# Kernel optimization log

Measured on AMD Instinct MI355X. Metric: run time of the kernel, lower is better.

The kernel has to match this reference:

```python
import jax, jax.numpy as jnp
import numpy as np

B, S, E, H = 2, 2048, 1024, 16
D = E // H  # dim per head


def setup_inputs() -> dict:
    key = jax.random.key(0)
    ks = jax.random.split(key, 13)
    sc = 1.0 / np.sqrt(E)
    inp = {
        "query": jax.random.normal(ks[0], (B, S, E), jnp.float32),
        "key": jax.random.normal(ks[1], (B, S, E), jnp.float32),
        "value": jax.random.normal(ks[2], (B, S, E), jnp.float32),
        "mask": jax.random.randint(ks[3], (B, S, S), 0, 2, jnp.int32),
        "Wq": jax.random.normal(ks[4], (E, E), jnp.float32) * sc,
        "bq": jnp.zeros((E,), jnp.float32),
        "Wk": jax.random.normal(ks[5], (E, E), jnp.float32) * sc,
        "bk": jnp.zeros((E,), jnp.float32),
        "Wv": jax.random.normal(ks[6], (E, E), jnp.float32) * sc,
        "bv": jnp.zeros((E,), jnp.float32),
        "Wo": jax.random.normal(ks[7], (E, E), jnp.float32) * sc,
        "bo": jnp.zeros((E,), jnp.float32),
    }
    return inp


def _split_heads(x):
    # [B, S, E] -> [B, H, S, D]
    return x.reshape(B, S, H, D).transpose(0, 2, 1, 3)


def reference(query, key, value, mask, Wq, bq, Wk, bk, Wv, bv, Wo, bo):
    q = _split_heads(query @ Wq.T + bq)
    k = _split_heads(key @ Wk.T + bk)
    v = _split_heads(value @ Wv.T + bv)

    dk = k.shape[-1]
    # scores: [B, H, Sq, Sk]
    scores = jnp.einsum("bhqd,bhkd->bhqk", q / jnp.sqrt(jnp.asarray(dk, q.dtype)), k)
    # mask broadcast over heads: [B, 1, Sq, Sk]; masked positions get -1e9
    scores = jnp.where(mask[:, None, :, :] == 0, jnp.asarray(-1e9, scores.dtype), scores)
    # fp32 softmax (dropout is identity in eval mode)
    attn = jax.nn.softmax(scores.astype(jnp.float32), axis=-1).astype(q.dtype)
    out = jnp.einsum("bhqk,bhkd->bhqd", attn, v)
    out = out.transpose(0, 2, 1, 3).reshape(B, S, E)
    return out @ Wo.T + bo
```

## Files before the change

kernel.cpp:

```cpp
#include <hip/hip_runtime.h>
#include <hip/hip_bf16.h>
#include <stdint.h>


typedef __bf16 bf16x8 __attribute__((ext_vector_type(8)));
typedef __bf16 bf16x4 __attribute__((ext_vector_type(4)));
typedef float  f32x4  __attribute__((ext_vector_type(4)));
typedef unsigned int u32x4 __attribute__((ext_vector_type(4)));

#define MFMA16(a, b, c) __builtin_amdgcn_mfma_f32_16x16x32_bf16((a), (b), (c), 0, 0, 0)

#if __has_builtin(__builtin_amdgcn_exp2f)
#define EXP2(x) __builtin_amdgcn_exp2f(x)
#else
#define EXP2(x) exp2f(x)
#endif

static constexpr int kB = 2, kS = 2048, kE = 1024, kH = 16, kD = 64;
static constexpr int kM = kB * kS;
static constexpr int kMaskWordsPerRow = kS / 64;
static constexpr float kLog2e = 1.4426950408889634f;

__device__ __forceinline__ void gload_lds16(const void* g, void* l) {
  __builtin_amdgcn_global_load_lds(
      (const __attribute__((address_space(1))) unsigned int*)g,
      (__attribute__((address_space(3))) unsigned int*)l, 16, 0, 0);
}

__device__ __forceinline__ unsigned pack_bf16x2(float a, float b) {
  unsigned short lo = __builtin_bit_cast(unsigned short, (__bf16)a);
  unsigned short hi = __builtin_bit_cast(unsigned short, (__bf16)b);
  return (unsigned)lo | ((unsigned)hi << 16);
}

static constexpr int kCvtBlocks = 1664;

__global__ __launch_bounds__(256) void cvt_pack_kernel(
    const float* __restrict__ q, const float* __restrict__ k, const float* __restrict__ v,
    const float* __restrict__ wq, const float* __restrict__ wk,
    const float* __restrict__ wv, const float* __restrict__ wo,
    const int* __restrict__ mask,
    __bf16* __restrict__ qb, __bf16* __restrict__ kb, __bf16* __restrict__ vb,
    __bf16* __restrict__ wqb, __bf16* __restrict__ wkb,
    __bf16* __restrict__ wvb, __bf16* __restrict__ wob,
    unsigned long long* __restrict__ mw) {
  const int bid = blockIdx.x;
  if (bid < 1216) {
    const float* src; __bf16* dst; int n8, t0, stride;
    if (bid < 960) {
      const int seg = bid / 320, sb = bid - seg * 320;
      src = (seg == 0) ? q : (seg == 1) ? k : v;
      dst = (seg == 0) ? qb : (seg == 1) ? kb : vb;
      n8 = (kM * kE) >> 3;
      t0 = sb * 256 + threadIdx.x;
      stride = 320 * 256;
    } else {
      const int wseg = (bid - 960) >> 6, sb = (bid - 960) & 63;
      src = (wseg == 0) ? wq : (wseg == 1) ? wk : (wseg == 2) ? wv : wo;
      dst = (wseg == 0) ? wqb : (wseg == 1) ? wkb : (wseg == 2) ? wvb : wob;
      n8 = (kE * kE) >> 3;
      t0 = sb * 256 + threadIdx.x;
      stride = 64 * 256;
    }
    for (int i = t0; i < n8; i += stride) {
      float4 f0 = ((const float4*)src)[2 * i];
      float4 f1 = ((const float4*)src)[2 * i + 1];
      bf16x8 o = {(__bf16)f0.x, (__bf16)f0.y, (__bf16)f0.z, (__bf16)f0.w,
                  (__bf16)f1.x, (__bf16)f1.y, (__bf16)f1.z, (__bf16)f1.w};
      ((bf16x8*)dst)[i] = o;
    }
    return;
  }
  const int lane = threadIdx.x & 63;
  const int wid = ((bid - 1216) * 4 + (threadIdx.x >> 6));
  const int nwords = kB * kS * kMaskWordsPerRow;
  const int stride4 = 1792 * 4;
  for (int w = wid * 4; w < nwords; w += stride4) {
    const int v0 = mask[(size_t)(w + 0) * 64 + lane];
    const int v1 = mask[(size_t)(w + 1) * 64 + lane];
    const int v2 = mask[(size_t)(w + 2) * 64 + lane];
    const int v3 = mask[(size_t)(w + 3) * 64 + lane];
    const unsigned long long b0 = __ballot(v0 != 0);
    const unsigned long long b1 = __ballot(v1 != 0);
    const unsigned long long b2 = __ballot(v2 != 0);
    const unsigned long long b3 = __ballot(v3 != 0);
    if (lane == 0) {
      ulonglong2 lo = {b0, b1}, hi = {b2, b3};
      *(ulonglong2*)&mw[w] = lo;
      *(ulonglong2*)&mw[w + 2] = hi;
    }
  }
}

__global__ __launch_bounds__(256) void gemm_bt(
    const __bf16* __restrict__ A0, const __bf16* __restrict__ A1, const __bf16* __restrict__ A2,
    const __bf16* __restrict__ W0, const __bf16* __restrict__ W1, const __bf16* __restrict__ W2,
    const float* __restrict__ b0, const float* __restrict__ b1, const float* __restrict__ b2,
    __bf16* __restrict__ O0, __bf16* __restrict__ O1, __bf16* __restrict__ O2) {
  const int z = blockIdx.z;
  const __bf16* A = (z == 0) ? A0 : (z == 1) ? A1 : A2;
  const __bf16* W = (z == 0) ? W0 : (z == 1) ? W1 : W2;
  const float* bias = (z == 0) ? b0 : (z == 1) ? b1 : b2;
  __bf16* OutB = (z == 0) ? O0 : (z == 1) ? O1 : O2;
  const float scale = (z == 0) ? 0.125f * kLog2e : 1.0f;

  const int n0 = blockIdx.x * 128;
  const int m0 = blockIdx.y * 128;
  const int tid = threadIdx.x;
  const int wave = tid >> 6, lane = tid & 63;
  const int g = lane >> 4, qi = lane & 15;
  const int wm = wave >> 1, wn = wave & 1;

  __shared__ __align__(16) __bf16 As[128 * 32];
  __shared__ __align__(16) __bf16 Bs[128 * 32];
  __shared__ __align__(16) __bf16 Ts[64 * 136];

  f32x4 acc[4][4];
#pragma unroll
  for (int i = 0; i < 4; ++i)
#pragma unroll
    for (int jj = 0; jj < 4; ++jj) acc[i][jj] = (f32x4){0.f, 0.f, 0.f, 0.f};

  for (int k0 = 0; k0 < kE; k0 += 32) {
#pragma unroll
    for (int jj = 0; jj < 2; ++jj) {
      const int c = jj * 256 + tid;
      const int r = c >> 2, sl = c & 3;
      gload_lds16(&A[(size_t)(m0 + r) * kE + k0 + sl * 8], &As[c * 8]);
      gload_lds16(&W[(size_t)(n0 + r) * kE + k0 + sl * 8], &Bs[c * 8]);
    }
    __syncthreads();

    bf16x8 af[4], bfr[4];
#pragma unroll
    for (int mi = 0; mi < 4; ++mi)
      af[mi] = *(const bf16x8*)&As[(wm * 64 + mi * 16 + qi) * 32 + g * 8];
#pragma unroll
    for (int nj = 0; nj < 4; ++nj)
      bfr[nj] = *(const bf16x8*)&Bs[(wn * 64 + nj * 16 + qi) * 32 + g * 8];
#pragma unroll
    for (int mi = 0; mi < 4; ++mi)
#pragma unroll
      for (int nj = 0; nj < 4; ++nj)
        acc[mi][nj] = MFMA16(af[mi], bfr[nj], acc[mi][nj]);
    __syncthreads();
  }

  if (z == 2) {
    const int bb = m0 >> 11, ss0 = m0 & 2047;
#pragma unroll
    for (int half = 0; half < 2; ++half) {
      __syncthreads();
      if (wn == half) {
#pragma unroll
        for (int nj = 0; nj < 4; ++nj) {
          const int dl = nj * 16 + qi;
          const float bn = bias[n0 + half * 64 + dl];
#pragma unroll
          for (int mi = 0; mi < 4; ++mi) {
            const int srow = wm * 64 + mi * 16 + g * 4;
            bf16x4 o;
#pragma unroll
            for (int r = 0; r < 4; ++r) o[r] = (__bf16)(acc[mi][nj][r] + bn);
            *(bf16x4*)&Ts[dl * 136 + srow] = o;
          }
        }
      }
      __syncthreads();
      const int drow = tid >> 2, sc = (tid & 3) * 32;
      const int head = (n0 + half * 64) >> 6;
      __bf16* dst = OutB + (((size_t)bb * kH + head) * kD + drow) * kS + ss0 + sc;
#pragma unroll
      for (int jj = 0; jj < 4; ++jj) {
        bf16x8 vv = *(const bf16x8*)&Ts[drow * 136 + sc + jj * 8];
        *(bf16x8*)&dst[jj * 8] = vv;
      }
    }
    return;
  }

#pragma unroll
  for (int nj = 0; nj < 4; ++nj) {
    const int ncol = n0 + wn * 64 + nj * 16 + qi;
    const float bn = bias[ncol];
    const int hh = ncol >> 6, dd = ncol & 63;
#pragma unroll
    for (int mi = 0; mi < 4; ++mi) {
#pragma unroll
      for (int r = 0; r < 4; ++r) {
        const int mrow = m0 + wm * 64 + mi * 16 + g * 4 + r;
        const float vv = (acc[mi][nj][r] + bn) * scale;
        const int bb = mrow >> 11, ss = mrow & 2047;
        OutB[((((size_t)bb * kH + hh) * kS + ss) << 6) + dd] = (__bf16)vv;
      }
    }
  }
}

__global__ __launch_bounds__(256) void gemm_out64(
    const __bf16* __restrict__ A, const __bf16* __restrict__ W,
    const float* __restrict__ bias, float* __restrict__ OF) {
  const int n0 = blockIdx.x * 64;
  const int m0 = blockIdx.y * 128;
  const int tid = threadIdx.x;
  const int wave = tid >> 6, lane = tid & 63;
  const int g = lane >> 4, qi = lane & 15;
  const int wm = wave >> 1, wn = wave & 1;

  __shared__ __align__(16) __bf16 As[128 * 32];
  __shared__ __align__(16) __bf16 Bs[64 * 32];

  f32x4 acc[4][2];
#pragma unroll
  for (int i = 0; i < 4; ++i)
#pragma unroll
    for (int jj = 0; jj < 2; ++jj) acc[i][jj] = (f32x4){0.f, 0.f, 0.f, 0.f};

  for (int k0 = 0; k0 < kE; k0 += 32) {
#pragma unroll
    for (int jj = 0; jj < 2; ++jj) {
      const int c = jj * 256 + tid;
      const int r = c >> 2, sl = c & 3;
      gload_lds16(&A[(size_t)(m0 + r) * kE + k0 + sl * 8], &As[c * 8]);
    }
    {
      const int r = tid >> 2, sl = tid & 3;
      gload_lds16(&W[(size_t)(n0 + r) * kE + k0 + sl * 8], &Bs[tid * 8]);
    }
    __syncthreads();

    bf16x8 af[4], bfr[2];
#pragma unroll
    for (int mi = 0; mi < 4; ++mi)
      af[mi] = *(const bf16x8*)&As[(wm * 64 + mi * 16 + qi) * 32 + g * 8];
#pragma unroll
    for (int nj = 0; nj < 2; ++nj)
      bfr[nj] = *(const bf16x8*)&Bs[(wn * 32 + nj * 16 + qi) * 32 + g * 8];
#pragma unroll
    for (int mi = 0; mi < 4; ++mi)
#pragma unroll
      for (int nj = 0; nj < 2; ++nj)
        acc[mi][nj] = MFMA16(af[mi], bfr[nj], acc[mi][nj]);
    __syncthreads();
  }

#pragma unroll
  for (int nj = 0; nj < 2; ++nj) {
    const int ncol = n0 + wn * 32 + nj * 16 + qi;
    const float bn = bias[ncol];
#pragma unroll
    for (int mi = 0; mi < 4; ++mi)
#pragma unroll
      for (int r = 0; r < 4; ++r) {
        const int mrow = m0 + wm * 64 + mi * 16 + g * 4 + r;
        OF[(size_t)mrow * kE + ncol] = acc[mi][nj][r] + bn;
      }
  }
}

__global__ __launch_bounds__(512, 4) void attn_kernel(
    const __bf16* __restrict__ Qh, const __bf16* __restrict__ Kh,
    const __bf16* __restrict__ Vt, const unsigned long long* __restrict__ mw,
    __bf16* __restrict__ Ob) {
  const int tid = threadIdx.x;
  const int wave = tid >> 6, lane = tid & 63;
  const int g = lane >> 4, qi = lane & 15;
  const int id = blockIdx.x;
  const int xcd = id & 7, j = id >> 3;
  const int bh = xcd * 4 + (j >> 4);
  const int qb = j & 15;
  const int b = bh >> 4, h = bh & 15;

  __shared__ __align__(16) __bf16 Ks[2][128 * 64];
  __shared__ __align__(16) __bf16 Vs[2][64 * 128];

  const __bf16* Qp = Qh + (size_t)bh * kS * kD;
  const __bf16* Kp = Kh + (size_t)bh * kS * kD;
  const __bf16* Vp = Vt + (size_t)bh * kD * kS;

  const int q0 = qb * 128 + wave * 16 + qi;
  const unsigned long long* M0 = mw + (size_t)(b * kS + q0) * kMaskWordsPerRow;

  const bf16x8 qf0 = *(const bf16x8*)&Qp[(size_t)q0 * kD + g * 8];
  const bf16x8 qf1 = *(const bf16x8*)&Qp[(size_t)q0 * kD + 32 + g * 8];

  f32x4 acc[4];
#pragma unroll
  for (int f = 0; f < 4; ++f) acc[f] = (f32x4){0.f, 0.f, 0.f, 0.f};
  float den = 0.f;
  const float ninf = __builtin_bit_cast(float, 0xff800000u);

  auto stage = [&](int buf, int kv0) {
#pragma unroll
    for (int jj = 0; jj < 2; ++jj) {
      const int c = jj * 512 + tid;
      const int kr = c >> 3, ksl = c & 7;
      gload_lds16(&Kp[(size_t)(kv0 + kr) * kD + (ksl ^ (kr & 7)) * 8],
                  &Ks[buf][c * 8]);
      const int vr = c >> 4, vsl = c & 15;
      gload_lds16(&Vp[(size_t)vr * kS + kv0 + (vsl ^ (vr & 7)) * 8],
                  &Vs[buf][c * 8]);
    }
  };

  stage(0, 0);
  __syncthreads();

  const int sw = qi & 7;
  for (int t = 0; t < 16; ++t) {
    const int cur = t & 1;
    if (t < 15) stage(cur ^ 1, (t + 1) * 128);
    const ulonglong2 wpair = *(const ulonglong2*)&M0[2 * t];
#pragma unroll
    for (int u = 0; u < 2; ++u) {
      const unsigned long long w = u ? wpair.y : wpair.x;
      const unsigned wlo = (unsigned)(w >> (g * 4));
      const unsigned whi = (unsigned)(w >> (32 + g * 4));
      const unsigned wf[4] = {wlo, wlo >> 16, whi, whi >> 16};

      float p[16];
      __builtin_amdgcn_s_setprio(1);
#pragma unroll
      for (int f = 0; f < 4; ++f) {
        const int r = u * 64 + f * 16 + qi;
        const bf16x8 k0 = *(const bf16x8*)&Ks[cur][r * 64 + ((g ^ sw) * 8)];
        const bf16x8 k1 = *(const bf16x8*)&Ks[cur][r * 64 + (((4 + g) ^ sw) * 8)];
        f32x4 st = (f32x4){0.f, 0.f, 0.f, 0.f};
        st = MFMA16(k0, qf0, st);
        st = MFMA16(k1, qf1, st);
#pragma unroll
        for (int r4 = 0; r4 < 4; ++r4)
          p[4 * f + r4] = (wf[f] & (1u << r4)) ? st[r4] : ninf;
      }
      __builtin_amdgcn_s_setprio(0);

#pragma unroll
      for (int i = 0; i < 16; ++i) {
        p[i] = EXP2(p[i]);
        den += p[i];
      }

      unsigned pk[4][2];
#pragma unroll
      for (int f = 0; f < 4; ++f) {
        pk[f][0] = pack_bf16x2(p[4 * f + 0], p[4 * f + 1]);
        pk[f][1] = pack_bf16x2(p[4 * f + 2], p[4 * f + 3]);
      }
#pragma unroll
      for (int c = 0; c < 2; ++c) {
        unsigned bw[4];
#pragma unroll
        for (int t4 = 0; t4 < 4; ++t4) {
          const int src = qi + 16 * ((t4 >> 1) + 2 * (g & 1));
          const int vA = __shfl((int)pk[2 * c + 0][t4 & 1], src);
          const int vB = __shfl((int)pk[2 * c + 1][t4 & 1], src);
          bw[t4] = (g >= 2) ? (unsigned)vB : (unsigned)vA;
        }
        const u32x4 tmp = {bw[0], bw[1], bw[2], bw[3]};
        const bf16x8 pb = __builtin_bit_cast(bf16x8, tmp);
        __builtin_amdgcn_s_setprio(1);
#pragma unroll
        for (int f = 0; f < 4; ++f) {
          const int rd = f * 16 + qi;
          const int slot = (u * 8 + c * 4 + g) ^ sw;
          const bf16x8 vfr = *(const bf16x8*)&Vs[cur][rd * 128 + slot * 8];
          acc[f] = MFMA16(vfr, pb, acc[f]);
        }
        __builtin_amdgcn_s_setprio(0);
      }
    }
    __syncthreads();
  }

  den += __shfl_xor(den, 16);
  den += __shfl_xor(den, 32);
  const float rinv = 1.0f / den;
  __bf16* Op = Ob + (size_t)(b * kS + q0) * kE + h * kD;
#pragma unroll
  for (int f = 0; f < 4; ++f) {
    ushort4 o;
    o.x = __builtin_bit_cast(unsigned short, (__bf16)(acc[f][0] * rinv));
    o.y = __builtin_bit_cast(unsigned short, (__bf16)(acc[f][1] * rinv));
    o.z = __builtin_bit_cast(unsigned short, (__bf16)(acc[f][2] * rinv));
    o.w = __builtin_bit_cast(unsigned short, (__bf16)(acc[f][3] * rinv));
    *(ushort4*)&Op[f * 16 + g * 4] = o;
  }
}

extern "C" void kernel_launch(void* const* d_in, const int* in_sizes, int n_in,
                              void* d_out, int out_size, void* d_ws, size_t ws_size,
                              hipStream_t stream) {
  (void)in_sizes; (void)n_in; (void)out_size; (void)ws_size;
  const float* q  = (const float*)d_in[0];
  const float* k  = (const float*)d_in[1];
  const float* v  = (const float*)d_in[2];
  const int*   mask = (const int*)d_in[3];
  const float* Wq = (const float*)d_in[4];
  const float* bq = (const float*)d_in[5];
  const float* Wk = (const float*)d_in[6];
  const float* bk = (const float*)d_in[7];
  const float* Wv = (const float*)d_in[8];
  const float* bv = (const float*)d_in[9];
  const float* Wo = (const float*)d_in[10];
  const float* bo = (const float*)d_in[11];

  char* ws = (char*)d_ws;
  const size_t MB = 1024 * 1024;
  __bf16* qb  = (__bf16*)(ws + 0 * MB);
  __bf16* kb  = (__bf16*)(ws + 8 * MB);
  __bf16* vb  = (__bf16*)(ws + 16 * MB);
  __bf16* wqb = (__bf16*)(ws + 24 * MB);
  __bf16* wkb = (__bf16*)(ws + 26 * MB);
  __bf16* wvb = (__bf16*)(ws + 28 * MB);
  __bf16* wob = (__bf16*)(ws + 30 * MB);
  __bf16* Qh  = (__bf16*)(ws + 32 * MB);
  __bf16* Kh  = (__bf16*)(ws + 40 * MB);
  __bf16* Vt  = (__bf16*)(ws + 48 * MB);
  unsigned long long* mwords = (unsigned long long*)(ws + 56 * MB);
  __bf16* Ob = qb;

  cvt_pack_kernel<<<kCvtBlocks, 256, 0, stream>>>(
      q, k, v, Wq, Wk, Wv, Wo, mask, qb, kb, vb, wqb, wkb, wvb, wob, mwords);
  gemm_bt<<<dim3(8, 32, 3), 256, 0, stream>>>(qb, kb, vb, wqb, wkb, wvb,
                                              bq, bk, bv, Qh, Kh, Vt);
  attn_kernel<<<512, 512, 0, stream>>>(Qh, Kh, Vt, mwords, Ob);
  gemm_out64<<<dim3(16, 32), 256, 0, stream>>>(Ob, wob, bo, (float*)d_out);
}
```

Baseline: 285.9 us.

## Process two query tiles per wave in attention and stage Q/K projection stores via LDS

The attention kernel now runs 256 threads per block, with each wave handling 32 query rows as two 16-row tiles. Each K/V fragment read from LDS is therefore reused for two sets of MFMAs, and KV is staged in 64-column double-buffered chunks. The softmax denominator is now accumulated with an MFMA against a ones vector instead of scalar adds and cross-lane shuffles. Separately, the Q/K projection epilogue writes through an LDS tile so the head-split output can be stored with coalesced 16-byte writes. The trade-off is higher register pressure per wave and fewer waves per block.

```diff
diff --git a/kernel.cpp b/kernel.cpp
--- a/kernel.cpp
+++ b/kernel.cpp
@@ -113,7 +113,7 @@
 
   __shared__ __align__(16) __bf16 As[128 * 32];
   __shared__ __align__(16) __bf16 Bs[128 * 32];
-  __shared__ __align__(16) __bf16 Ts[64 * 136];
+  __shared__ __align__(16) __bf16 Ts[128 * 72];
 
   f32x4 acc[4][4];
 #pragma unroll
@@ -146,8 +146,8 @@
     __syncthreads();
   }
 
+  const int bb = m0 >> 11, ss0 = m0 & 2047;
   if (z == 2) {
-    const int bb = m0 >> 11, ss0 = m0 & 2047;
 #pragma unroll
     for (int half = 0; half < 2; ++half) {
       __syncthreads();
@@ -180,20 +180,30 @@
   }
 
 #pragma unroll
-  for (int nj = 0; nj < 4; ++nj) {
-    const int ncol = n0 + wn * 64 + nj * 16 + qi;
-    const float bn = bias[ncol];
-    const int hh = ncol >> 6, dd = ncol & 63;
-#pragma unroll
-    for (int mi = 0; mi < 4; ++mi) {
-#pragma unroll
-      for (int r = 0; r < 4; ++r) {
-        const int mrow = m0 + wm * 64 + mi * 16 + g * 4 + r;
-        const float vv = (acc[mi][nj][r] + bn) * scale;
-        const int bb = mrow >> 11, ss = mrow & 2047;
-        OutB[((((size_t)bb * kH + hh) * kS + ss) << 6) + dd] = (__bf16)vv;
+  for (int half = 0; half < 2; ++half) {
+    __syncthreads();
+    if (wn == half) {
+#pragma unroll
+      for (int nj = 0; nj < 4; ++nj) {
+        const int dl = nj * 16 + qi;
+        const float bn = bias[n0 + half * 64 + dl];
+#pragma unroll
+        for (int mi = 0; mi < 4; ++mi) {
+          const int srow = wm * 64 + mi * 16 + g * 4;
+#pragma unroll
+          for (int r = 0; r < 4; ++r)
+            Ts[(srow + r) * 72 + dl] = (__bf16)((acc[mi][nj][r] + bn) * scale);
+        }
       }
     }
+    __syncthreads();
+    const int row = tid >> 1, cg = tid & 1;
+    const int head = (n0 + half * 64) >> 6;
+    __bf16* dst =
+        OutB + (((size_t)bb * kH + head) * kS + ss0 + row) * kD + cg * 32;
+#pragma unroll
+    for (int jj = 0; jj < 4; ++jj)
+      *(bf16x8*)&dst[jj * 8] = *(const bf16x8*)&Ts[row * 72 + cg * 32 + jj * 8];
   }
 }
 
@@ -258,7 +268,7 @@
   }
 }
 
-__global__ __launch_bounds__(512, 4) void attn_kernel(
+__global__ __launch_bounds__(256, 2) void attn_kernel(
     const __bf16* __restrict__ Qh, const __bf16* __restrict__ Kh,
     const __bf16* __restrict__ Vt, const unsigned long long* __restrict__ mw,
     __bf16* __restrict__ Ob) {
@@ -271,119 +281,160 @@
   const int qb = j & 15;
   const int b = bh >> 4, h = bh & 15;
 
-  __shared__ __align__(16) __bf16 Ks[2][128 * 64];
-  __shared__ __align__(16) __bf16 Vs[2][64 * 128];
+  __shared__ __align__(16) __bf16 Ks[2][64 * 64];
+  __shared__ __align__(16) __bf16 Vs[2][64 * 64];
 
   const __bf16* Qp = Qh + (size_t)bh * kS * kD;
   const __bf16* Kp = Kh + (size_t)bh * kS * kD;
   const __bf16* Vp = Vt + (size_t)bh * kD * kS;
 
-  const int q0 = qb * 128 + wave * 16 + qi;
+  const int q0 = qb * 128 + wave * 32 + qi;
+  const int q1 = q0 + 16;
   const unsigned long long* M0 = mw + (size_t)(b * kS + q0) * kMaskWordsPerRow;
-
-  const bf16x8 qf0 = *(const bf16x8*)&Qp[(size_t)q0 * kD + g * 8];
-  const bf16x8 qf1 = *(const bf16x8*)&Qp[(size_t)q0 * kD + 32 + g * 8];
-
-  f32x4 acc[4];
-#pragma unroll
-  for (int f = 0; f < 4; ++f) acc[f] = (f32x4){0.f, 0.f, 0.f, 0.f};
-  float den = 0.f;
+  const unsigned long long* M1 = mw + (size_t)(b * kS + q1) * kMaskWordsPerRow;
+
+  const bf16x8 qf00 = *(const bf16x8*)&Qp[(size_t)q0 * kD + g * 8];
+  const bf16x8 qf01 = *(const bf16x8*)&Qp[(size_t)q0 * kD + 32 + g * 8];
+  const bf16x8 qf10 = *(const bf16x8*)&Qp[(size_t)q1 * kD + g * 8];
+  const bf16x8 qf11 = *(const bf16x8*)&Qp[(size_t)q1 * kD + 32 + g * 8];
+
+  f32x4 acc0[4], acc1[4];
+#pragma unroll
+  for (int f = 0; f < 4; ++f) {
+    acc0[f] = (f32x4){0.f, 0.f, 0.f, 0.f};
+    acc1[f] = (f32x4){0.f, 0.f, 0.f, 0.f};
+  }
+  f32x4 accd0 = (f32x4){0.f, 0.f, 0.f, 0.f};
+  f32x4 accd1 = (f32x4){0.f, 0.f, 0.f, 0.f};
+  const f32x4 kZero = (f32x4){0.f, 0.f, 0.f, 0.f};
   const float ninf = __builtin_bit_cast(float, 0xff800000u);
+  const u32x4 onesu = {0x3F803F80u, 0x3F803F80u, 0x3F803F80u, 0x3F803F80u};
+  const bf16x8 vones = __builtin_bit_cast(bf16x8, onesu);
+
+  const int sw = qi & 7;
+  const char* kA = (const char*)&Ks[0][0] + (qi * 64 + ((g ^ sw) * 8)) * 2;
+  const char* kBp = (const char*)&Ks[0][0] + (qi * 64 + (((4 + g) ^ sw) * 8)) * 2;
+  const char* vA = (const char*)&Vs[0][0] + (qi * 64 + ((g ^ sw) * 8)) * 2;
+  const char* vB = (const char*)&Vs[0][0] + (qi * 64 + (((4 + g) ^ sw) * 8)) * 2;
 
   auto stage = [&](int buf, int kv0) {
 #pragma unroll
     for (int jj = 0; jj < 2; ++jj) {
-      const int c = jj * 512 + tid;
-      const int kr = c >> 3, ksl = c & 7;
-      gload_lds16(&Kp[(size_t)(kv0 + kr) * kD + (ksl ^ (kr & 7)) * 8],
-                  &Ks[buf][c * 8]);
-      const int vr = c >> 4, vsl = c & 15;
-      gload_lds16(&Vp[(size_t)vr * kS + kv0 + (vsl ^ (vr & 7)) * 8],
-                  &Vs[buf][c * 8]);
+      const int c = jj * 256 + tid;
+      const int row = c >> 3, sl = c & 7;
+      const int sls = sl ^ (row & 7);
+      gload_lds16(&Kp[(size_t)(kv0 + row) * kD + sls * 8], &Ks[buf][c * 8]);
+      gload_lds16(&Vp[(size_t)row * kS + kv0 + sls * 8], &Vs[buf][c * 8]);
     }
   };
+
+#define ATTN_BODY(BUF, W0, W1)                                                 \
+  {                                                                            \
+    const unsigned long long w0_ = (W0), w1_ = (W1);                           \
+    unsigned wf0_[4], wf1_[4];                                                 \
+    {                                                                          \
+      const unsigned lo0 = (unsigned)(w0_ >> (g * 4));                         \
+      const unsigned hi0 = (unsigned)(w0_ >> (32 + g * 4));                    \
+      wf0_[0] = lo0; wf0_[1] = lo0 >> 16; wf0_[2] = hi0; wf0_[3] = hi0 >> 16;  \
+      const unsigned lo1 = (unsigned)(w1_ >> (g * 4));                         \
+      const unsigned hi1 = (unsigned)(w1_ >> (32 + g * 4));                    \
+      wf1_[0] = lo1; wf1_[1] = lo1 >> 16; wf1_[2] = hi1; wf1_[3] = hi1 >> 16;  \
+    }                                                                          \
+    float p0_[16], p1_[16];                                                    \
+    __builtin_amdgcn_s_setprio(1);                                             \
+    _Pragma("unroll")                                                          \
+    for (int f = 0; f < 4; ++f) {                                              \
+      const bf16x8 k0_ = *(const bf16x8*)(kA + (BUF)*8192 + f * 2048);         \
+      const bf16x8 k1_ = *(const bf16x8*)(kBp + (BUF)*8192 + f * 2048);        \
+      f32x4 st0_ = MFMA16(k0_, qf00, kZero);                                   \
+      st0_ = MFMA16(k1_, qf01, st0_);                                          \
+      f32x4 st1_ = MFMA16(k0_, qf10, kZero);                                   \
+      st1_ = MFMA16(k1_, qf11, st1_);                                          \
+      _Pragma("unroll")                                                        \
+      for (int r4 = 0; r4 < 4; ++r4) {                                         \
+        p0_[4 * f + r4] = (wf0_[f] & (1u << r4)) ? st0_[r4] : ninf;            \
+        p1_[4 * f + r4] = (wf1_[f] & (1u << r4)) ? st1_[r4] : ninf;            \
+      }                                                                        \
+    }                                                                          \
+    __builtin_amdgcn_s_setprio(0);                                             \
+    _Pragma("unroll")                                                          \
+    for (int i = 0; i < 16; ++i) {                                             \
+      p0_[i] = EXP2(p0_[i]);                                                   \
+      p1_[i] = EXP2(p1_[i]);                                                   \
+    }                                                                          \
+    unsigned pk0_[4][2], pk1_[4][2];                                           \
+    _Pragma("unroll")                                                          \
+    for (int f = 0; f < 4; ++f) {                                              \
+      pk0_[f][0] = pack_bf16x2(p0_[4 * f + 0], p0_[4 * f + 1]);                \
+      pk0_[f][1] = pack_bf16x2(p0_[4 * f + 2], p0_[4 * f + 3]);                \
+      pk1_[f][0] = pack_bf16x2(p1_[4 * f + 0], p1_[4 * f + 1]);                \
+      pk1_[f][1] = pack_bf16x2(p1_[4 * f + 2], p1_[4 * f + 3]);                \
+    }                                                                          \
+    _Pragma("unroll")                                                          \
+    for (int c = 0; c < 2; ++c) {                                              \
+      unsigned bw0_[4], bw1_[4];                                               \
+      _Pragma("unroll")                                                        \
+      for (int t4 = 0; t4 < 4; ++t4) {                                         \
+        const int src_ = qi + 16 * ((t4 >> 1) + 2 * (g & 1));                  \
+        const int a0_ = __shfl((int)pk0_[2 * c + 0][t4 & 1], src_);            \
+        const int b0_ = __shfl((int)pk0_[2 * c + 1][t4 & 1], src_);            \
+        bw0_[t4] = (g >= 2) ? (unsigned)b0_ : (unsigned)a0_;                   \
+        const int a1_ = __shfl((int)pk1_[2 * c + 0][t4 & 1], src_);            \
+        const int b1_ = __shfl((int)pk1_[2 * c + 1][t4 & 1], src_);            \
+        bw1_[t4] = (g >= 2) ? (unsigned)b1_ : (unsigned)a1_;                   \
+      }                                                                        \
+      const u32x4 u0_ = {bw0_[0], bw0_[1], bw0_[2], bw0_[3]};                  \
+      const u32x4 u1_ = {bw1_[0], bw1_[1], bw1_[2], bw1_[3]};                  \
+      const bf16x8 pb0_ = __builtin_bit_cast(bf16x8, u0_);                     \
+      const bf16x8 pb1_ = __builtin_bit_cast(bf16x8, u1_);                     \
+      __builtin_amdgcn_s_setprio(1);                                           \
+      _Pragma("unroll")                                                        \
+      for (int f = 0; f < 4; ++f) {                                            \
+        const bf16x8 vf_ = (c == 0)                                            \
+            ? *(const bf16x8*)(vA + (BUF)*8192 + f * 2048)                     \
+            : *(const bf16x8*)(vB + (BUF)*8192 + f * 2048);                    \
+        acc0[f] = MFMA16(vf_, pb0_, acc0[f]);                                  \
+        acc1[f] = MFMA16(vf_, pb1_, acc1[f]);                                  \
+      }                                                                        \
+      accd0 = MFMA16(vones, pb0_, accd0);                                      \
+      accd1 = MFMA16(vones, pb1_, accd1);                                      \
+      __builtin_amdgcn_s_setprio(0);                                           \
+    }                                                                          \
+  }
 
   stage(0, 0);
   __syncthreads();
 
-  const int sw = qi & 7;
-  for (int t = 0; t < 16; ++t) {
-    const int cur = t & 1;
-    if (t < 15) stage(cur ^ 1, (t + 1) * 128);
-    const ulonglong2 wpair = *(const ulonglong2*)&M0[2 * t];
-#pragma unroll
-    for (int u = 0; u < 2; ++u) {
-      const unsigned long long w = u ? wpair.y : wpair.x;
-      const unsigned wlo = (unsigned)(w >> (g * 4));
-      const unsigned whi = (unsigned)(w >> (32 + g * 4));
-      const unsigned wf[4] = {wlo, wlo >> 16, whi, whi >> 16};
-
-      float p[16];
-      __builtin_amdgcn_s_setprio(1);
-#pragma unroll
-      for (int f = 0; f < 4; ++f) {
-        const int r = u * 64 + f * 16 + qi;
-        const bf16x8 k0 = *(const bf16x8*)&Ks[cur][r * 64 + ((g ^ sw) * 8)];
-        const bf16x8 k1 = *(const bf16x8*)&Ks[cur][r * 64 + (((4 + g) ^ sw) * 8)];
-        f32x4 st = (f32x4){0.f, 0.f, 0.f, 0.f};
-        st = MFMA16(k0, qf0, st);
-        st = MFMA16(k1, qf1, st);
-#pragma unroll
-        for (int r4 = 0; r4 < 4; ++r4)
-          p[4 * f + r4] = (wf[f] & (1u << r4)) ? st[r4] : ninf;
-      }
-      __builtin_amdgcn_s_setprio(0);
-
-#pragma unroll
-      for (int i = 0; i < 16; ++i) {
-        p[i] = EXP2(p[i]);
-        den += p[i];
-      }
-
-      unsigned pk[4][2];
-#pragma unroll
-      for (int f = 0; f < 4; ++f) {
-        pk[f][0] = pack_bf16x2(p[4 * f + 0], p[4 * f + 1]);
-        pk[f][1] = pack_bf16x2(p[4 * f + 2], p[4 * f + 3]);
-      }
-#pragma unroll
-      for (int c = 0; c < 2; ++c) {
-        unsigned bw[4];
-#pragma unroll
-        for (int t4 = 0; t4 < 4; ++t4) {
-          const int src = qi + 16 * ((t4 >> 1) + 2 * (g & 1));
-          const int vA = __shfl((int)pk[2 * c + 0][t4 & 1], src);
-          const int vB = __shfl((int)pk[2 * c + 1][t4 & 1], src);
-          bw[t4] = (g >= 2) ? (unsigned)vB : (unsigned)vA;
-        }
-        const u32x4 tmp = {bw[0], bw[1], bw[2], bw[3]};
-        const bf16x8 pb = __builtin_bit_cast(bf16x8, tmp);
-        __builtin_amdgcn_s_setprio(1);
-#pragma unroll
-        for (int f = 0; f < 4; ++f) {
-          const int rd = f * 16 + qi;
-          const int slot = (u * 8 + c * 4 + g) ^ sw;
-          const bf16x8 vfr = *(const bf16x8*)&Vs[cur][rd * 128 + slot * 8];
-          acc[f] = MFMA16(vfr, pb, acc[f]);
-        }
-        __builtin_amdgcn_s_setprio(0);
-      }
-    }
-    __syncthreads();
-  }
-
-  den += __shfl_xor(den, 16);
-  den += __shfl_xor(den, 32);
-  const float rinv = 1.0f / den;
-  __bf16* Op = Ob + (size_t)(b * kS + q0) * kE + h * kD;
+#pragma unroll 1
+  for (int tt = 0; tt < 16; ++tt) {
+    const ulonglong2 w0p = *(const ulonglong2*)&M0[2 * tt];
+    const ulonglong2 w1p = *(const ulonglong2*)&M1[2 * tt];
+    stage(1, (2 * tt + 1) * 64);
+    ATTN_BODY(0, w0p.x, w1p.x);
+    __syncthreads();
+    if (tt < 15) stage(0, (2 * tt + 2) * 64);
+    ATTN_BODY(1, w0p.y, w1p.y);
+    __syncthreads();
+  }
+#undef ATTN_BODY
+
+  const float ri0 = 1.0f / accd0[0];
+  const float ri1 = 1.0f / accd1[0];
+  __bf16* Op0 = Ob + (size_t)(b * kS + q0) * kE + h * kD;
+  __bf16* Op1 = Ob + (size_t)(b * kS + q1) * kE + h * kD;
 #pragma unroll
   for (int f = 0; f < 4; ++f) {
-    ushort4 o;
-    o.x = __builtin_bit_cast(unsigned short, (__bf16)(acc[f][0] * rinv));
-    o.y = __builtin_bit_cast(unsigned short, (__bf16)(acc[f][1] * rinv));
-    o.z = __builtin_bit_cast(unsigned short, (__bf16)(acc[f][2] * rinv));
-    o.w = __builtin_bit_cast(unsigned short, (__bf16)(acc[f][3] * rinv));
-    *(ushort4*)&Op[f * 16 + g * 4] = o;
+    ushort4 o0, o1;
+    o0.x = __builtin_bit_cast(unsigned short, (__bf16)(acc0[f][0] * ri0));
+    o0.y = __builtin_bit_cast(unsigned short, (__bf16)(acc0[f][1] * ri0));
+    o0.z = __builtin_bit_cast(unsigned short, (__bf16)(acc0[f][2] * ri0));
+    o0.w = __builtin_bit_cast(unsigned short, (__bf16)(acc0[f][3] * ri0));
+    *(ushort4*)&Op0[f * 16 + g * 4] = o0;
+    o1.x = __builtin_bit_cast(unsigned short, (__bf16)(acc1[f][0] * ri1));
+    o1.y = __builtin_bit_cast(unsigned short, (__bf16)(acc1[f][1] * ri1));
+    o1.z = __builtin_bit_cast(unsigned short, (__bf16)(acc1[f][2] * ri1));
+    o1.w = __builtin_bit_cast(unsigned short, (__bf16)(acc1[f][3] * ri1));
+    *(ushort4*)&Op1[f * 16 + g * 4] = o1;
   }
 }
 
@@ -423,6 +474,6 @@
       q, k, v, Wq, Wk, Wv, Wo, mask, qb, kb, vb, wqb, wkb, wvb, wob, mwords);
   gemm_bt<<<dim3(8, 32, 3), 256, 0, stream>>>(qb, kb, vb, wqb, wkb, wvb,
                                               bq, bk, bv, Qh, Kh, Vt);
-  attn_kernel<<<512, 512, 0, stream>>>(Qh, Kh, Vt, mwords, Ob);
+  attn_kernel<<<512, 256, 0, stream>>>(Qh, Kh, Vt, mwords, Ob);
   gemm_out64<<<dim3(16, 32), 256, 0, stream>>>(Ob, wob, bo, (float*)d_out);
 }
```

Result: faster. 277.9 us (-2.8%).
